# Kernel optimization log

Measured on AMD Instinct MI355X. Metric: run time of the kernel, lower is better.

The kernel has to match this reference:

```python
import jax, jax.numpy as jnp
import numpy as np

N, E, D, H, C = 50000, 800000, 128, 128, 40
EPS = 1e-5


def setup_inputs() -> dict:
    key = jax.random.key(0)
    ks = jax.random.split(key, 18)
    s = lambda d: 1.0 / np.sqrt(d)
    inp = {
        "x": jax.random.normal(ks[0], (N, D), dtype=jnp.float32),
        "edge_index": jax.random.randint(ks[1], (2, E), 0, N, dtype=jnp.int64),
        # GCNConv weights (x @ W + b after normalized aggregation)
        "W1": jax.random.normal(ks[2], (D, H), dtype=jnp.float32) * s(D),
        "b1": jax.random.normal(ks[3], (H,), dtype=jnp.float32) * 0.01,
        "W2": jax.random.normal(ks[4], (H, H), dtype=jnp.float32) * s(H),
        "b2": jax.random.normal(ks[5], (H,), dtype=jnp.float32) * 0.01,
        "W3": jax.random.normal(ks[6], (H, H), dtype=jnp.float32) * s(H),
        "b3": jax.random.normal(ks[7], (H,), dtype=jnp.float32) * 0.01,
        # LayerNorm params (applied after layers 0 and 1 only)
        "ln1_g": 1.0 + 0.1 * jax.random.normal(ks[8], (H,), dtype=jnp.float32),
        "ln1_b": 0.1 * jax.random.normal(ks[9], (H,), dtype=jnp.float32),
        "ln2_g": 1.0 + 0.1 * jax.random.normal(ks[10], (H,), dtype=jnp.float32),
        "ln2_b": 0.1 * jax.random.normal(ks[11], (H,), dtype=jnp.float32),
        # post_mp MLP head
        "mpW1": jax.random.normal(ks[12], (H, H), dtype=jnp.float32) * s(H),
        "mpb1": jax.random.normal(ks[13], (H,), dtype=jnp.float32) * 0.01,
        "mpW2": jax.random.normal(ks[14], (H, C), dtype=jnp.float32) * s(H),
        "mpb2": jax.random.normal(ks[15], (C,), dtype=jnp.float32) * 0.01,
    }
    return inp


def _layernorm(h, g, b):
    mu = jnp.mean(h, axis=-1, keepdims=True)
    var = jnp.mean((h - mu) ** 2, axis=-1, keepdims=True)
    return (h - mu) * jax.lax.rsqrt(var + EPS) * g + b


def _gcn_forward(x, edge_index, params):
    (W1, b1, W2, b2, W3, b3, ln1_g, ln1_b, ln2_g, ln2_b, mpW1, mpb1, mpW2, mpb2) = params
    n = x.shape[0]
    loop = jnp.arange(n, dtype=edge_index.dtype)
    src = jnp.concatenate([edge_index[0], loop])  # source-to-target flow + self-loops
    dst = jnp.concatenate([edge_index[1], loop])
    deg = jax.ops.segment_sum(jnp.ones_like(src, dtype=x.dtype), dst, num_segments=n)
    dis = jax.lax.rsqrt(deg)  # deg >= 1 due to self-loops
    norm = dis[src] * dis[dst]  # [E+N]

    def conv(h, W, b):
        h = h @ W
        msg = h[src] * norm[:, None]  # gather + scale
        return jax.ops.segment_sum(msg, dst, num_segments=n) + b  # scatter-add

    h = x
    # layer 0
    h = conv(h, W1, b1)
    h = jax.nn.relu(h)  # dropout p=0.1 -> identity in eval
    h = _layernorm(h, ln1_g, ln1_b)
    # layer 1
    h = conv(h, W2, b2)
    h = jax.nn.relu(h)
    h = _layernorm(h, ln2_g, ln2_b)
    # layer 2 (emb is pre-relu conv output)
    emb = conv(h, W3, b3)
    h = jax.nn.relu(emb)
    # post_mp: Linear -> Dropout(eval: identity) -> Linear
    h = h @ mpW1 + mpb1
    logits = h @ mpW2 + mpb2
    return emb, jax.nn.log_softmax(logits, axis=1)


def reference(x, edge_index, W1, b1, W2, b2, W3, b3, ln1_g, ln1_b, ln2_g, ln2_b, mpW1, mpb1, mpW2, mpb2):
    params = (W1, b1, W2, b2, W3, b3, ln1_g, ln1_b, ln2_g, ln2_b, mpW1, mpb1, mpW2, mpb2)
    return _gcn_forward(x, edge_index, params)
```

## Files before the change

kernel.cpp:

```cpp
#include <hip/hip_runtime.h>

typedef __bf16 bf16x8 __attribute__((ext_vector_type(8)));
typedef float  f32x4  __attribute__((ext_vector_type(4)));
typedef float  f32x2  __attribute__((ext_vector_type(2)));
typedef unsigned short u16;
typedef unsigned int   u32;
typedef long long      i64;

#define BSH  7
#define BCAP 4096
#define NPB  256

__device__ __forceinline__ float b2f(u16 x){ return __uint_as_float(((u32)x) << 16); }
__device__ __forceinline__ u16 f2b(float x){
  u32 u = __float_as_uint(x);
  return (u16)((u + 0x7FFFu + ((u >> 16) & 1u)) >> 16);
}

__device__ __forceinline__ void d2acc(u32 pair, f32x2& a){
  f32x2 t;
  t.x = __uint_as_float(pair << 16);
  t.y = __uint_as_float(pair & 0xFFFF0000u);
  a += t;
}
__device__ __forceinline__ void acc8(uint4 q, f32x2* a){
  d2acc(q.x, a[0]); d2acc(q.y, a[1]); d2acc(q.z, a[2]); d2acc(q.w, a[3]);
}

__global__ __launch_bounds__(256) void k_detect(const u16* __restrict__ x,
                                                const u32* __restrict__ ei,
                                                int* __restrict__ flags,
                                                u16* __restrict__ T, int n){
  __shared__ int sh[2];
  int t = threadIdx.x;
  if (t < 2) sh[t] = 0;
  __syncthreads();
  int sane = 0;
  for (int i = t; i < 4096; i += 256){
    u16 u = x[i]; u32 e = (u >> 7) & 0xFFu;
    if (u == 0 || (e >= 0x70u && e <= 0x8Fu)) sane++;
  }
  int nz = 0;
  for (int i = t; i < 1024; i += 256)
    if (ei[2*i + 1] != 0u) nz++;
  atomicAdd(&sh[0], sane);
  atomicAdd(&sh[1], nz);
  if (t < 128) T[(size_t)n*128 + t] = 0;
  else         T[(size_t)n*128 + t] = 0;
  __syncthreads();
  if (t == 0){
    flags[0] = (sh[0] < 3500) ? 1 : 0;
    flags[1] = (sh[1] == 0) ? 1 : 0;
  }
}

__device__ __forceinline__ int ld_idx(const void* ei, long long j, int is64){
  return is64 ? (int)((const i64*)ei)[j] : ((const int*)ei)[j];
}
__device__ __forceinline__ void ld8(const void* p, int base, int f, float* o){
  if (f){
    float4 a = *(const float4*)((const float*)p + base);
    float4 b = *(const float4*)((const float*)p + base + 4);
    o[0]=a.x; o[1]=a.y; o[2]=a.z; o[3]=a.w;
    o[4]=b.x; o[5]=b.y; o[6]=b.z; o[7]=b.w;
  } else {
    uint4 q = *(const uint4*)((const u16*)p + base);
    o[0]=b2f((u16)(q.x&0xffff)); o[1]=b2f((u16)(q.x>>16));
    o[2]=b2f((u16)(q.y&0xffff)); o[3]=b2f((u16)(q.y>>16));
    o[4]=b2f((u16)(q.z&0xffff)); o[5]=b2f((u16)(q.z>>16));
    o[6]=b2f((u16)(q.w&0xffff)); o[7]=b2f((u16)(q.w>>16));
  }
}

__global__ __launch_bounds__(256) void k_partA(const void* __restrict__ ei, int E, int n,
                                               int* __restrict__ cntmat,
                                               const int* __restrict__ flags, int nbuk){
  __shared__ int cnt[512];
  int t = threadIdx.x;
  int is64 = flags[1];
  for (int i = t; i < 512; i += 256) cnt[i] = 0;
  __syncthreads();
  long long R = ((long long)E + NPB - 1) / NPB;
  long long lo = (long long)blockIdx.x * R;
  long long hi = lo + R; if (hi > E) hi = E;
  for (long long e = lo + t; e < hi; e += 256){
    int d = ld_idx(ei, (long long)E + e, is64);
    if ((unsigned)d < (unsigned)n) atomicAdd(&cnt[(unsigned)d >> BSH], 1);
  }
  __syncthreads();
  for (int b = t; b < nbuk; b += 256)
    cntmat[(size_t)b*NPB + blockIdx.x] = cnt[b];
}

__global__ __launch_bounds__(NPB) void k_scanBK(const int* __restrict__ cntmat,
                                                int* __restrict__ basemat,
                                                int* __restrict__ bcnt){
  __shared__ int sh[NPB];
  int b = blockIdx.x, t = threadIdx.x;
  int v = cntmat[(size_t)b*NPB + t];
  sh[t] = v; __syncthreads();
  for (int off = 1; off < NPB; off <<= 1){
    int u = 0; if (t >= off) u = sh[t - off];
    __syncthreads(); sh[t] += u; __syncthreads();
  }
  basemat[(size_t)b*NPB + t] = sh[t] - v;
  if (t == NPB-1) bcnt[b] = sh[t];
}

__global__ __launch_bounds__(256) void k_partC(const void* __restrict__ ei, int E, int n,
                                               const int* __restrict__ basemat,
                                               u32* __restrict__ ebuf,
                                               const int* __restrict__ flags, int nbuk){
  __shared__ int cur[512];
  int t = threadIdx.x;
  int is64 = flags[1];
  for (int i = t; i < 512; i += 256) cur[i] = 0;
  __syncthreads();
  for (int b = t; b < nbuk; b += 256) cur[b] = basemat[(size_t)b*NPB + blockIdx.x];
  __syncthreads();
  long long R = ((long long)E + NPB - 1) / NPB;
  long long lo = (long long)blockIdx.x * R;
  long long hi = lo + R; if (hi > E) hi = E;
  for (long long e = lo + t; e < hi; e += 256){
    int d = ld_idx(ei, (long long)E + e, is64);
    int s = ld_idx(ei, e, is64);
    if ((unsigned)d < (unsigned)n && (unsigned)s < (unsigned)n){
      int b = (unsigned)d >> BSH;
      int p = atomicAdd(&cur[b], 1);
      if (p < BCAP) ebuf[(size_t)b*BCAP + p] = (u32)s | ((u32)(d & ((1<<BSH)-1)) << 17);
    }
  }
}

__global__ __launch_bounds__(256) void k_bdeg(const int* __restrict__ bcnt,
                                              const u32* __restrict__ ebuf,
                                              int* __restrict__ deg, int n){
  __shared__ int cnt[1<<BSH];
  int b = blockIdx.x, t = threadIdx.x;
  if (t < (1<<BSH)) cnt[t] = 0;
  __syncthreads();
  int m = bcnt[b]; if (m > BCAP) m = BCAP;
  const u32* eb = ebuf + (size_t)b*BCAP;
  for (int i = t; i < m; i += 256)
    atomicAdd(&cnt[eb[i] >> 17], 1);
  __syncthreads();
  if (t < (1<<BSH)){
    int node = (b << BSH) + t;
    if (node < n) deg[node] = cnt[t];
  }
}

__global__ __launch_bounds__(256) void k_scanA(const int* __restrict__ deg, int n,
                                               int* __restrict__ bsum){
  __shared__ int sh[256];
  int t = threadIdx.x;
  int base = blockIdx.x*1024 + t*4;
  int s = 0;
  #pragma unroll
  for (int i = 0; i < 4; ++i){
    int idx = base + i;
    if (idx < n) s += (deg[idx] + 3) & ~3;
  }
  sh[t] = s; __syncthreads();
  for (int off = 128; off; off >>= 1){
    if (t < off) sh[t] += sh[t + off];
    __syncthreads();
  }
  if (t == 0) bsum[blockIdx.x] = sh[0];
}

__global__ __launch_bounds__(256) void k_scanB(int* __restrict__ bsum, int nB,
                                               int* __restrict__ rowptr, int n){
  __shared__ int sh[256];
  int t = threadIdx.x;
  int v = (t < nB) ? bsum[t] : 0;
  sh[t] = v; __syncthreads();
  for (int off = 1; off < 256; off <<= 1){
    int u = 0; if (t >= off) u = sh[t - off];
    __syncthreads(); sh[t] += u; __syncthreads();
  }
  if (t < nB) bsum[t] = sh[t] - v;
  if (t == 255) rowptr[n] = sh[255];
}

__global__ __launch_bounds__(256) void k_scanC(const int* __restrict__ deg, int n,
                                               const int* __restrict__ bsum,
                                               int* __restrict__ rowptr,
                                               float* __restrict__ dis){
  __shared__ int sh[256];
  int t = threadIdx.x;
  int base = blockIdx.x*1024 + t*4;
  int d[4]; int s = 0;
  #pragma unroll
  for (int i = 0; i < 4; ++i){
    int idx = base + i;
    d[i] = (idx < n) ? deg[idx] : 0;
    s += (d[i] + 3) & ~3;
  }
  sh[t] = s; __syncthreads();
  for (int off = 1; off < 256; off <<= 1){
    int u = 0; if (t >= off) u = sh[t - off];
    __syncthreads(); sh[t] += u; __syncthreads();
  }
  int run = bsum[blockIdx.x] + sh[t] - s;
  #pragma unroll
  for (int i = 0; i < 4; ++i){
    int idx = base + i;
    if (idx < n){
      rowptr[idx] = run; run += (d[i] + 3) & ~3;
      dis[idx] = rsqrtf((float)(d[i] + 1));
    }
  }
}

__global__ __launch_bounds__(256) void k_bfill(const int* __restrict__ bcnt,
                                               const u32* __restrict__ ebuf,
                                               const int* __restrict__ rowptr,
                                               int* __restrict__ colx, int n){
  __shared__ int cur[1<<BSH];
  int b = blockIdx.x, t = threadIdx.x;
  int node = (b << BSH) + (t & ((1<<BSH)-1));
  if (t < (1<<BSH))
    cur[t] = (node < n) ? rowptr[node] : 0;
  __syncthreads();
  int m = bcnt[b]; if (m > BCAP) m = BCAP;
  const u32* eb = ebuf + (size_t)b*BCAP;
  for (int i = t; i < m; i += 256){
    u32 e = eb[i];
    int p = atomicAdd(&cur[e >> 17], 1);
    colx[p] = (int)((e & 0x1FFFFu) << 8);
  }
  __syncthreads();
  if (t < (1<<BSH) && node < n){
    int zoff = n << 8;
    int end = rowptr[node + 1];
    for (int p = cur[t]; p < end; ++p) colx[p] = zoff;
  }
}

__global__ __launch_bounds__(64) void k_shufW3(const void* __restrict__ W1,
                                               const void* __restrict__ W2,
                                               const void* __restrict__ W3,
                                               u16* __restrict__ Ws,
                                               const int* __restrict__ flags){
  int f = flags[0];
  int sel = blockIdx.x >> 5;
  const void* W = (sel == 0) ? W1 : (sel == 1) ? W2 : W3;
  u16* Wo = Ws + (size_t)sel * 128 * 128;
  int bid = blockIdx.x & 31;
  int nt = bid >> 2, kk = bid & 3;
  int l = threadIdx.x;
  int g = l >> 4, mr = l & 15;
  int nn = nt*16 + mr;
  #pragma unroll
  for (int i = 0; i < 8; ++i){
    int k = kk*32 + g*4 + (i & 3) + ((i >> 2) << 4);
    u16 w = f ? f2b(((const float*)W)[k*128 + nn]) : ((const u16*)W)[k*128 + nn];
    Wo[(size_t)(bid*64 + l)*8 + i] = w;
  }
}

__global__ __launch_bounds__(256) void k_gemm(const void* __restrict__ A, int aExt,
    const u16* __restrict__ Ws, const float* __restrict__ dis,
    u16* __restrict__ T, int nTiles, const int* __restrict__ flags)
{
  int wave = threadIdx.x >> 6, lane = threadIdx.x & 63;
  int tile = blockIdx.x*4 + wave;
  if (tile >= nTiles) return;
  int g = lane >> 4, mr = lane & 15;
  int f = aExt ? flags[0] : 0;
  union U8 { ushort4 q[2]; u16 s[8]; bf16x8 b; };
  bf16x8 a[4];
  if (f){
    const float* ap = (const float*)A + (size_t)(tile*16 + mr)*128;
    #pragma unroll
    for (int kk = 0; kk < 4; ++kk){
      float4 p = *(const float4*)(ap + kk*32 + g*4);
      float4 q = *(const float4*)(ap + kk*32 + g*4 + 16);
      U8 u;
      u.s[0]=f2b(p.x); u.s[1]=f2b(p.y); u.s[2]=f2b(p.z); u.s[3]=f2b(p.w);
      u.s[4]=f2b(q.x); u.s[5]=f2b(q.y); u.s[6]=f2b(q.z); u.s[7]=f2b(q.w);
      a[kk] = u.b;
    }
  } else {
    const u16* ap = (const u16*)A + (size_t)(tile*16 + mr)*128;
    #pragma unroll
    for (int kk = 0; kk < 4; ++kk){
      U8 u;
      u.q[0] = *(const ushort4*)(ap + kk*32 + g*4);
      u.q[1] = *(const ushort4*)(ap + kk*32 + g*4 + 16);
      a[kk] = u.b;
    }
  }
  float dj[4];
  #pragma unroll
  for (int j = 0; j < 4; ++j) dj[j] = dis[tile*16 + g*4 + j];
  #pragma unroll
  for (int nt = 0; nt < 8; ++nt){
    f32x4 acc = {0.f,0.f,0.f,0.f};
    #pragma unroll
    for (int kk = 0; kk < 4; ++kk){
      bf16x8 b = *(const bf16x8*)(Ws + (size_t)((nt*4 + kk)*64 + lane)*8);
      acc = __builtin_amdgcn_mfma_f32_16x16x32_bf16(a[kk], b, acc, 0, 0, 0);
    }
    int nn = nt*16 + mr;
    #pragma unroll
    for (int j = 0; j < 4; ++j){
      int row = tile*16 + g*4 + j;
      T[(size_t)row*128 + nn] = f2b(acc[j] * dj[j]);
    }
  }
}

template<int MODE>
__global__ __launch_bounds__(256) void k_agg(const u16* __restrict__ T,
    const int* __restrict__ rowptr, const int* __restrict__ colx,
    const float* __restrict__ dis, const void* __restrict__ bias,
    const void* __restrict__ lg, const void* __restrict__ lb,
    void* __restrict__ outA, int n, const int* __restrict__ flags)
{
  int wave = threadIdx.x >> 6, l = threadIdx.x & 63;
  int g = l >> 4, c = l & 15;
  int v = blockIdx.x*16 + wave*4 + g;
  bool alive = v < n;
  int vv = alive ? v : (n - 1);
  int f = flags[0];
  const char* Tb = (const char*)T + c*16;

  f32x2 aA[4] = {};
  f32x2 aB[4] = {};
  {
    uint4 q = *(const uint4*)(Tb + ((size_t)vv << 8));
    acc8(q, aA);
  }
  int s = rowptr[vv], e = rowptr[vv+1];
  int i = s;
  for (; i + 8 <= e; i += 8){
    uint4 oA = *(const uint4*)(colx + i);
    uint4 oB = *(const uint4*)(colx + i + 4);
    uint4 q0 = *(const uint4*)(Tb + oA.x);
    uint4 q1 = *(const uint4*)(Tb + oA.y);
    uint4 q2 = *(const uint4*)(Tb + oA.z);
    uint4 q3 = *(const uint4*)(Tb + oA.w);
    uint4 q4 = *(const uint4*)(Tb + oB.x);
    uint4 q5 = *(const uint4*)(Tb + oB.y);
    uint4 q6 = *(const uint4*)(Tb + oB.z);
    uint4 q7 = *(const uint4*)(Tb + oB.w);
    acc8(q0, aA); acc8(q1, aB); acc8(q2, aA); acc8(q3, aB);
    acc8(q4, aA); acc8(q5, aB); acc8(q6, aA); acc8(q7, aB);
  }
  if (i < e){
    uint4 o = *(const uint4*)(colx + i);
    uint4 q0 = *(const uint4*)(Tb + o.x);
    uint4 q1 = *(const uint4*)(Tb + o.y);
    uint4 q2 = *(const uint4*)(Tb + o.z);
    uint4 q3 = *(const uint4*)(Tb + o.w);
    acc8(q0, aA); acc8(q1, aB); acc8(q2, aA); acc8(q3, aB);
  }

  float acc[8];
  #pragma unroll
  for (int k = 0; k < 4; ++k){
    acc[2*k]   = aA[k].x + aB[k].x;
    acc[2*k+1] = aA[k].y + aB[k].y;
  }
  float sc = dis[vv];
  float bv[8]; ld8(bias, c*8, f, bv);
  float x[8];
  #pragma unroll
  for (int k = 0; k < 8; ++k) x[k] = fmaf(acc[k], sc, bv[k]);

  if (MODE == 0){
    #pragma unroll
    for (int k = 0; k < 8; ++k) x[k] = fmaxf(x[k], 0.f);
    float sum = 0.f;
    #pragma unroll
    for (int k = 0; k < 8; ++k) sum += x[k];
    #pragma unroll
    for (int off = 8; off; off >>= 1) sum += __shfl_xor(sum, off);
    float mu = sum * (1.f/128.f);
    float vs = 0.f;
    #pragma unroll
    for (int k = 0; k < 8; ++k){ float d = x[k] - mu; vs += d*d; }
    #pragma unroll
    for (int off = 8; off; off >>= 1) vs += __shfl_xor(vs, off);
    float inv = rsqrtf(vs*(1.f/128.f) + 1e-5f);
    float gv[8], bvv[8];
    ld8(lg, c*8, f, gv); ld8(lb, c*8, f, bvv);
    if (alive){
      uint4 w;
      float y0,y1;
      y0 = (x[0]-mu)*inv*gv[0] + bvv[0]; y1 = (x[1]-mu)*inv*gv[1] + bvv[1];
      w.x = (u32)f2b(y0) | ((u32)f2b(y1) << 16);
      y0 = (x[2]-mu)*inv*gv[2] + bvv[2]; y1 = (x[3]-mu)*inv*gv[3] + bvv[3];
      w.y = (u32)f2b(y0) | ((u32)f2b(y1) << 16);
      y0 = (x[4]-mu)*inv*gv[4] + bvv[4]; y1 = (x[5]-mu)*inv*gv[5] + bvv[5];
      w.z = (u32)f2b(y0) | ((u32)f2b(y1) << 16);
      y0 = (x[6]-mu)*inv*gv[6] + bvv[6]; y1 = (x[7]-mu)*inv*gv[7] + bvv[7];
      w.w = (u32)f2b(y0) | ((u32)f2b(y1) << 16);
      *(uint4*)((u16*)outA + (size_t)v*128 + c*8) = w;
    }
  } else {
    if (alive){
      if (f){
        float* oa = (float*)outA + (size_t)v*128 + c*8;
        *(float4*)(oa)     = make_float4(x[0], x[1], x[2], x[3]);
        *(float4*)(oa + 4) = make_float4(x[4], x[5], x[6], x[7]);
      } else {
        uint4 w;
        w.x = (u32)f2b(x[0]) | ((u32)f2b(x[1]) << 16);
        w.y = (u32)f2b(x[2]) | ((u32)f2b(x[3]) << 16);
        w.z = (u32)f2b(x[4]) | ((u32)f2b(x[5]) << 16);
        w.w = (u32)f2b(x[6]) | ((u32)f2b(x[7]) << 16);
        *(uint4*)((u16*)outA + (size_t)v*128 + c*8) = w;
      }
    }
  }
}

__global__ __launch_bounds__(128) void k_wc(const void* __restrict__ mpW1, const void* __restrict__ mpb1,
    const void* __restrict__ mpW2, const void* __restrict__ mpb2,
    float* __restrict__ Wc, float* __restrict__ bc, const int* __restrict__ flags)
{
  int f = flags[0];
  int c = blockIdx.x;
  int k = threadIdx.x;
  float acc = 0.f;
  if (f){
    const float* A  = (const float*)mpW1 + (size_t)k*128;
    const float* B2 = (const float*)mpW2;
    #pragma unroll 8
    for (int j = 0; j < 128; ++j) acc = fmaf(A[j], B2[j*40 + c], acc);
    if (k == 0){
      const float* b1p = (const float*)mpb1;
      float b = ((const float*)mpb2)[c];
      #pragma unroll 8
      for (int j = 0; j < 128; ++j) b = fmaf(b1p[j], B2[j*40 + c], b);
      bc[c] = b;
    }
  } else {
    const u16* A  = (const u16*)mpW1 + (size_t)k*128;
    const u16* B2 = (const u16*)mpW2;
    #pragma unroll 8
    for (int j = 0; j < 128; ++j) acc = fmaf(b2f(A[j]), b2f(B2[j*40 + c]), acc);
    if (k == 0){
      const u16* b1p = (const u16*)mpb1;
      float b = b2f(((const u16*)mpb2)[c]);
      #pragma unroll 8
      for (int j = 0; j < 128; ++j) b = fmaf(b2f(b1p[j]), b2f(B2[j*40 + c]), b);
      bc[c] = b;
    }
  }
  Wc[k*40 + c] = acc;
}

__global__ __launch_bounds__(64) void k_shufWc(const float* __restrict__ Wc, u16* __restrict__ Wcs){
  int bid = blockIdx.x;
  int nt = bid >> 2, kk = bid & 3;
  int l = threadIdx.x;
  int g = l >> 4, mr = l & 15;
  int nn = nt*16 + mr;
  #pragma unroll
  for (int i = 0; i < 8; ++i){
    int k = kk*32 + g*4 + (i & 3) + ((i >> 2) << 4);
    Wcs[(size_t)(bid*64 + l)*8 + i] = (nn < 40) ? f2b(Wc[k*40 + nn]) : (u16)0;
  }
}

__global__ __launch_bounds__(256) void k_logitsM(const u16* __restrict__ Wcs,
    const float* __restrict__ bc, void* __restrict__ dout, int n,
    const int* __restrict__ flags)
{
  int wave = threadIdx.x >> 6, lane = threadIdx.x & 63;
  int tile = blockIdx.x*4 + wave;
  int nTiles = n >> 4;
  if (tile >= nTiles) return;
  int f = flags[0];
  int g = lane >> 4, mr = lane & 15;
  union U8 { ushort4 q[2]; u16 s[8]; bf16x8 b; };
  bf16x8 a[4];
  if (f){
    const float* ap = (const float*)dout + (size_t)(tile*16 + mr)*128;
    #pragma unroll
    for (int kk = 0; kk < 4; ++kk){
      float4 p = *(const float4*)(ap + kk*32 + g*4);
      float4 q = *(const float4*)(ap + kk*32 + g*4 + 16);
      U8 u;
      u.s[0]=f2b(fmaxf(p.x,0.f)); u.s[1]=f2b(fmaxf(p.y,0.f));
      u.s[2]=f2b(fmaxf(p.z,0.f)); u.s[3]=f2b(fmaxf(p.w,0.f));
      u.s[4]=f2b(fmaxf(q.x,0.f)); u.s[5]=f2b(fmaxf(q.y,0.f));
      u.s[6]=f2b(fmaxf(q.z,0.f)); u.s[7]=f2b(fmaxf(q.w,0.f));
      a[kk] = u.b;
    }
  } else {
    const u16* ap = (const u16*)dout + (size_t)(tile*16 + mr)*128;
    #pragma unroll
    for (int kk = 0; kk < 4; ++kk){
      U8 u;
      u.q[0] = *(const ushort4*)(ap + kk*32 + g*4);
      u.q[1] = *(const ushort4*)(ap + kk*32 + g*4 + 16);
      #pragma unroll
      for (int i = 0; i < 8; ++i) u.s[i] = (u.s[i] & 0x8000u) ? (u16)0 : u.s[i];
      a[kk] = u.b;
    }
  }
  f32x4 acc[3];
  #pragma unroll
  for (int nt = 0; nt < 3; ++nt){
    f32x4 c4 = {0.f,0.f,0.f,0.f};
    #pragma unroll
    for (int kk = 0; kk < 4; ++kk){
      bf16x8 b = *(const bf16x8*)(Wcs + (size_t)((nt*4 + kk)*64 + lane)*8);
      c4 = __builtin_amdgcn_mfma_f32_16x16x32_bf16(a[kk], b, c4, 0, 0, 0);
    }
    acc[nt] = c4;
  }
  float bcv[3]; bool valid[3];
  #pragma unroll
  for (int nt = 0; nt < 3; ++nt){
    int c = nt*16 + mr;
    valid[nt] = (c < 40);
    bcv[nt] = valid[nt] ? bc[c] : 0.f;
  }
  float* of = (float*)dout + (size_t)n*128;
  u16*  ob = (u16*) dout + (size_t)n*128;
  #pragma unroll
  for (int j = 0; j < 4; ++j){
    float l0 = valid[0] ? acc[0][j] + bcv[0] : -3.0e38f;
    float l1 = valid[1] ? acc[1][j] + bcv[1] : -3.0e38f;
    float l2 = valid[2] ? acc[2][j] + bcv[2] : -3.0e38f;
    float m = fmaxf(l0, fmaxf(l1, l2));
    #pragma unroll
    for (int off = 8; off; off >>= 1) m = fmaxf(m, __shfl_xor(m, off));
    float ssum = (valid[0] ? expf(l0 - m) : 0.f)
               + (valid[1] ? expf(l1 - m) : 0.f)
               + (valid[2] ? expf(l2 - m) : 0.f);
    #pragma unroll
    for (int off = 8; off; off >>= 1) ssum += __shfl_xor(ssum, off);
    float lgs = m + logf(ssum);
    int node = tile*16 + g*4 + j;
    #pragma unroll
    for (int nt = 0; nt < 3; ++nt){
      if (valid[nt]){
        int c = nt*16 + mr;
        float r = (nt==0 ? l0 : (nt==1 ? l1 : l2)) - lgs;
        if (f) of[(size_t)node*40 + c] = r;
        else   ob[(size_t)node*40 + c] = f2b(r);
      }
    }
  }
}

extern "C" void kernel_launch(void* const* d_in, const int* in_sizes, int n_in,
                              void* d_out, int out_size, void* d_ws, size_t ws_size,
                              hipStream_t stream)
{
  const int n = in_sizes[0] / 128;
  const int E = in_sizes[1] / 2;

  const void* x    = d_in[0];
  const void* ei   = d_in[1];
  const void* W1   = d_in[2];
  const void* b1   = d_in[3];
  const void* W2   = d_in[4];
  const void* b2   = d_in[5];
  const void* W3   = d_in[6];
  const void* b3   = d_in[7];
  const void* ln1g = d_in[8];
  const void* ln1b = d_in[9];
  const void* ln2g = d_in[10];
  const void* ln2b = d_in[11];
  const void* mpW1 = d_in[12];
  const void* mpb1 = d_in[13];
  const void* mpW2 = d_in[14];
  const void* mpb2 = d_in[15];

  u16* Hbuf = (u16*)d_out;

  char* w = (char*)d_ws;
  size_t off = 0;
  auto alloc = [&](size_t bytes)->char*{
    char* p = w + off; off = (off + bytes + 255) & ~(size_t)255; return p;
  };
  const int nbuk = (n + (1<<BSH) - 1) >> BSH;

  int*   flags = (int*)  alloc(256);
  float* dis   = (float*)alloc((size_t)n*4);
  int*   deg   = (int*)  alloc((size_t)n*4);
  int*   rowp  = (int*)  alloc((size_t)(n+1)*4);
  int*   bsum  = (int*)  alloc(1024);
  int*   bcnt  = (int*)  alloc((size_t)nbuk*4);
  int*   cntm  = (int*)  alloc((size_t)nbuk*NPB*4);
  int*   basem = (int*)  alloc((size_t)nbuk*NPB*4);
  u32*   ebuf  = (u32*)  alloc((size_t)nbuk*BCAP*4);
  int*   colx  = (int*)  alloc(((size_t)E + 4*(size_t)n)*4 + 256);
  u16*   T     = (u16*)  alloc((size_t)(n+1)*128*2);
  u16*   Ws    = (u16*)  alloc((size_t)3*128*128*2);
  float* Wc    = (float*)alloc((size_t)128*40*4);
  float* bc    = (float*)alloc((size_t)64*4);
  u16*   Wcs   = (u16*)  alloc((size_t)12*64*8*2);

  int nB = (n + 1023) / 1024;

  k_detect<<<1, 256, 0, stream>>>((const u16*)x, (const u32*)ei, flags, T, n);
  k_shufW3<<<96, 64, 0, stream>>>(W1, W2, W3, Ws, flags);
  k_partA <<<NPB, 256, 0, stream>>>(ei, E, n, cntm, flags, nbuk);
  k_scanBK<<<nbuk, NPB, 0, stream>>>(cntm, basem, bcnt);
  k_partC <<<NPB, 256, 0, stream>>>(ei, E, n, basem, ebuf, flags, nbuk);
  k_bdeg  <<<nbuk, 256, 0, stream>>>(bcnt, ebuf, deg, n);
  k_scanA <<<nB, 256, 0, stream>>>(deg, n, bsum);
  k_scanB <<<1, 256, 0, stream>>>(bsum, nB, rowp, n);
  k_scanC <<<nB, 256, 0, stream>>>(deg, n, bsum, rowp, dis);
  k_bfill <<<nbuk, 256, 0, stream>>>(bcnt, ebuf, rowp, colx, n);
  k_wc    <<<40, 128, 0, stream>>>(mpW1, mpb1, mpW2, mpb2, Wc, bc, flags);
  k_shufWc<<<12, 64, 0, stream>>>(Wc, Wcs);

  int nTiles = (n + 15) / 16;
  int gG = (nTiles + 3) / 4;
  int gA = (n + 15) / 16;

  k_gemm <<<gG, 256, 0, stream>>>(x, 1, Ws, dis, T, nTiles, flags);
  k_agg<0><<<gA, 256, 0, stream>>>(T, rowp, colx, dis, b1, ln1g, ln1b, Hbuf, n, flags);
  k_gemm <<<gG, 256, 0, stream>>>(Hbuf, 0, Ws + (size_t)128*128, dis, T, nTiles, flags);
  k_agg<0><<<gA, 256, 0, stream>>>(T, rowp, colx, dis, b2, ln2g, ln2b, Hbuf, n, flags);
  k_gemm <<<gG, 256, 0, stream>>>(Hbuf, 0, Ws + (size_t)2*128*128, dis, T, nTiles, flags);
  k_agg<1><<<gA, 256, 0, stream>>>(T, rowp, colx, dis, b3, nullptr, nullptr, d_out, n, flags);
  k_logitsM<<<gG, 256, 0, stream>>>(Wcs, bc, d_out, n, flags);
}
```

Baseline: 213.3 us.

## Sub-bucket edges by source-node range to sort CSR columns by source

Edge partitioning now keys each edge by destination bucket and by a source-node range (8192-node tiles). The CSR column lists are therefore filled in roughly source-sorted order, which should give the aggregation gathers better locality across neighbouring rows. In exchange, the bucket count grows several-fold, so the scan needs more blocks and the count and fill kernels loop over sub-buckets, with one extra barrier per sub-bucket. The per-bucket capacity drops to 512, which risks dropping edges if a sub-bucket overflows.

```diff
diff --git a/kernel.cpp b/kernel.cpp
--- a/kernel.cpp
+++ b/kernel.cpp
@@ -7,9 +7,11 @@
 typedef unsigned int   u32;
 typedef long long      i64;
 
-#define BSH  7
-#define BCAP 4096
-#define NPB  256
+#define BSH   7
+#define SRCSH 13
+#define BCAP  512
+#define NPB   256
+#define MAXB2 4096
 
 __device__ __forceinline__ float b2f(u16 x){ return __uint_as_float(((u32)x) << 16); }
 __device__ __forceinline__ u16 f2b(float x){
@@ -46,7 +48,6 @@
   atomicAdd(&sh[0], sane);
   atomicAdd(&sh[1], nz);
   if (t < 128) T[(size_t)n*128 + t] = 0;
-  else         T[(size_t)n*128 + t] = 0;
   __syncthreads();
   if (t == 0){
     flags[0] = (sh[0] < 3500) ? 1 : 0;
@@ -74,21 +75,26 @@
 
 __global__ __launch_bounds__(256) void k_partA(const void* __restrict__ ei, int E, int n,
                                                int* __restrict__ cntmat,
-                                               const int* __restrict__ flags, int nbuk){
-  __shared__ int cnt[512];
+                                               const int* __restrict__ flags,
+                                               int NT, int nb2){
+  __shared__ int cnt[MAXB2];
   int t = threadIdx.x;
   int is64 = flags[1];
-  for (int i = t; i < 512; i += 256) cnt[i] = 0;
+  for (int i = t; i < nb2; i += 256) cnt[i] = 0;
   __syncthreads();
   long long R = ((long long)E + NPB - 1) / NPB;
   long long lo = (long long)blockIdx.x * R;
   long long hi = lo + R; if (hi > E) hi = E;
   for (long long e = lo + t; e < hi; e += 256){
     int d = ld_idx(ei, (long long)E + e, is64);
-    if ((unsigned)d < (unsigned)n) atomicAdd(&cnt[(unsigned)d >> BSH], 1);
-  }
-  __syncthreads();
-  for (int b = t; b < nbuk; b += 256)
+    int s = ld_idx(ei, e, is64);
+    if ((unsigned)d < (unsigned)n && (unsigned)s < (unsigned)n){
+      int key = ((unsigned)d >> BSH)*NT + ((unsigned)s >> SRCSH);
+      atomicAdd(&cnt[key], 1);
+    }
+  }
+  __syncthreads();
+  for (int b = t; b < nb2; b += 256)
     cntmat[(size_t)b*NPB + blockIdx.x] = cnt[b];
 }
 
@@ -110,13 +116,12 @@
 __global__ __launch_bounds__(256) void k_partC(const void* __restrict__ ei, int E, int n,
                                                const int* __restrict__ basemat,
                                                u32* __restrict__ ebuf,
-                                               const int* __restrict__ flags, int nbuk){
-  __shared__ int cur[512];
+                                               const int* __restrict__ flags,
+                                               int NT, int nb2){
+  __shared__ int cur[MAXB2];
   int t = threadIdx.x;
   int is64 = flags[1];
-  for (int i = t; i < 512; i += 256) cur[i] = 0;
-  __syncthreads();
-  for (int b = t; b < nbuk; b += 256) cur[b] = basemat[(size_t)b*NPB + blockIdx.x];
+  for (int b = t; b < nb2; b += 256) cur[b] = basemat[(size_t)b*NPB + blockIdx.x];
   __syncthreads();
   long long R = ((long long)E + NPB - 1) / NPB;
   long long lo = (long long)blockIdx.x * R;
@@ -125,24 +130,27 @@
     int d = ld_idx(ei, (long long)E + e, is64);
     int s = ld_idx(ei, e, is64);
     if ((unsigned)d < (unsigned)n && (unsigned)s < (unsigned)n){
-      int b = (unsigned)d >> BSH;
-      int p = atomicAdd(&cur[b], 1);
-      if (p < BCAP) ebuf[(size_t)b*BCAP + p] = (u32)s | ((u32)(d & ((1<<BSH)-1)) << 17);
+      int key = ((unsigned)d >> BSH)*NT + ((unsigned)s >> SRCSH);
+      int p = atomicAdd(&cur[key], 1);
+      if (p < BCAP) ebuf[(size_t)key*BCAP + p] = (u32)s | ((u32)(d & ((1<<BSH)-1)) << 17);
     }
   }
 }
 
 __global__ __launch_bounds__(256) void k_bdeg(const int* __restrict__ bcnt,
                                               const u32* __restrict__ ebuf,
-                                              int* __restrict__ deg, int n){
+                                              int* __restrict__ deg, int n, int NT){
   __shared__ int cnt[1<<BSH];
   int b = blockIdx.x, t = threadIdx.x;
   if (t < (1<<BSH)) cnt[t] = 0;
   __syncthreads();
-  int m = bcnt[b]; if (m > BCAP) m = BCAP;
-  const u32* eb = ebuf + (size_t)b*BCAP;
-  for (int i = t; i < m; i += 256)
-    atomicAdd(&cnt[eb[i] >> 17], 1);
+  for (int st = 0; st < NT; ++st){
+    int key = b*NT + st;
+    int m = bcnt[key]; if (m > BCAP) m = BCAP;
+    const u32* eb = ebuf + (size_t)key*BCAP;
+    for (int i = t; i < m; i += 256)
+      atomicAdd(&cnt[eb[i] >> 17], 1);
+  }
   __syncthreads();
   if (t < (1<<BSH)){
     int node = (b << BSH) + t;
@@ -216,21 +224,24 @@
 __global__ __launch_bounds__(256) void k_bfill(const int* __restrict__ bcnt,
                                                const u32* __restrict__ ebuf,
                                                const int* __restrict__ rowptr,
-                                               int* __restrict__ colx, int n){
+                                               int* __restrict__ colx, int n, int NT){
   __shared__ int cur[1<<BSH];
   int b = blockIdx.x, t = threadIdx.x;
   int node = (b << BSH) + (t & ((1<<BSH)-1));
   if (t < (1<<BSH))
     cur[t] = (node < n) ? rowptr[node] : 0;
   __syncthreads();
-  int m = bcnt[b]; if (m > BCAP) m = BCAP;
-  const u32* eb = ebuf + (size_t)b*BCAP;
-  for (int i = t; i < m; i += 256){
-    u32 e = eb[i];
-    int p = atomicAdd(&cur[e >> 17], 1);
-    colx[p] = (int)((e & 0x1FFFFu) << 8);
-  }
-  __syncthreads();
+  for (int st = 0; st < NT; ++st){
+    int key = b*NT + st;
+    int m = bcnt[key]; if (m > BCAP) m = BCAP;
+    const u32* eb = ebuf + (size_t)key*BCAP;
+    for (int i = t; i < m; i += 256){
+      u32 e = eb[i];
+      int p = atomicAdd(&cur[e >> 17], 1);
+      colx[p] = (int)((e & 0x1FFFFu) << 8);
+    }
+    __syncthreads();
+  }
   if (t < (1<<BSH) && node < n){
     int zoff = n << 8;
     int end = rowptr[node + 1];
@@ -583,16 +594,19 @@
     char* p = w + off; off = (off + bytes + 255) & ~(size_t)255; return p;
   };
   const int nbuk = (n + (1<<BSH) - 1) >> BSH;
+  int NT = (n + (1<<SRCSH) - 1) >> SRCSH;
+  int nb2 = nbuk * NT;
+  if (nb2 > MAXB2){ NT = MAXB2 / nbuk; nb2 = nbuk * NT; }
 
   int*   flags = (int*)  alloc(256);
   float* dis   = (float*)alloc((size_t)n*4);
   int*   deg   = (int*)  alloc((size_t)n*4);
   int*   rowp  = (int*)  alloc((size_t)(n+1)*4);
   int*   bsum  = (int*)  alloc(1024);
-  int*   bcnt  = (int*)  alloc((size_t)nbuk*4);
-  int*   cntm  = (int*)  alloc((size_t)nbuk*NPB*4);
-  int*   basem = (int*)  alloc((size_t)nbuk*NPB*4);
-  u32*   ebuf  = (u32*)  alloc((size_t)nbuk*BCAP*4);
+  int*   bcnt  = (int*)  alloc((size_t)nb2*4);
+  int*   cntm  = (int*)  alloc((size_t)nb2*NPB*4);
+  int*   basem = (int*)  alloc((size_t)nb2*NPB*4);
+  u32*   ebuf  = (u32*)  alloc((size_t)nb2*BCAP*4);
   int*   colx  = (int*)  alloc(((size_t)E + 4*(size_t)n)*4 + 256);
   u16*   T     = (u16*)  alloc((size_t)(n+1)*128*2);
   u16*   Ws    = (u16*)  alloc((size_t)3*128*128*2);
@@ -604,14 +618,14 @@
 
   k_detect<<<1, 256, 0, stream>>>((const u16*)x, (const u32*)ei, flags, T, n);
   k_shufW3<<<96, 64, 0, stream>>>(W1, W2, W3, Ws, flags);
-  k_partA <<<NPB, 256, 0, stream>>>(ei, E, n, cntm, flags, nbuk);
-  k_scanBK<<<nbuk, NPB, 0, stream>>>(cntm, basem, bcnt);
-  k_partC <<<NPB, 256, 0, stream>>>(ei, E, n, basem, ebuf, flags, nbuk);
-  k_bdeg  <<<nbuk, 256, 0, stream>>>(bcnt, ebuf, deg, n);
+  k_partA <<<NPB, 256, 0, stream>>>(ei, E, n, cntm, flags, NT, nb2);
+  k_scanBK<<<nb2, NPB, 0, stream>>>(cntm, basem, bcnt);
+  k_partC <<<NPB, 256, 0, stream>>>(ei, E, n, basem, ebuf, flags, NT, nb2);
+  k_bdeg  <<<nbuk, 256, 0, stream>>>(bcnt, ebuf, deg, n, NT);
   k_scanA <<<nB, 256, 0, stream>>>(deg, n, bsum);
   k_scanB <<<1, 256, 0, stream>>>(bsum, nB, rowp, n);
   k_scanC <<<nB, 256, 0, stream>>>(deg, n, bsum, rowp, dis);
-  k_bfill <<<nbuk, 256, 0, stream>>>(bcnt, ebuf, rowp, colx, n);
+  k_bfill <<<nbuk, 256, 0, stream>>>(bcnt, ebuf, rowp, colx, n, NT);
   k_wc    <<<40, 128, 0, stream>>>(mpW1, mpb1, mpW2, mpb2, Wc, bc, flags);
   k_shufWc<<<12, 64, 0, stream>>>(Wc, Wcs);
 
```

New measurement: 227.2 us. +6.5%, slower.

## Fold CSR prefix scan into bucket kernels and merge Wc shuffle

Applied to the files above, without the earlier changes.

Replaces the three-kernel scan over per-node degrees (scanA/scanB/scanC) with a per-bucket reduction inside k_bdeg, a single 512-thread bucket scan, and an intra-bucket scan inside k_bfill, which now also writes rowptr and dis. The Wc precompute writes the shuffled bf16 layout directly, which removes the separate k_shufWc launch and the intermediate buffer. The aim is to cut several small kernel launches and global round trips in the preprocessing chain. It relies on nbuk being at most 512 so the single-block scan is valid.

```diff
diff --git a/kernel.cpp b/kernel.cpp
--- a/kernel.cpp
+++ b/kernel.cpp
@@ -46,7 +46,6 @@
   atomicAdd(&sh[0], sane);
   atomicAdd(&sh[1], nz);
   if (t < 128) T[(size_t)n*128 + t] = 0;
-  else         T[(size_t)n*128 + t] = 0;
   __syncthreads();
   if (t == 0){
     flags[0] = (sh[0] < 3500) ? 1 : 0;
@@ -134,8 +133,10 @@
 
 __global__ __launch_bounds__(256) void k_bdeg(const int* __restrict__ bcnt,
                                               const u32* __restrict__ ebuf,
-                                              int* __restrict__ deg, int n){
+                                              int* __restrict__ deg,
+                                              int* __restrict__ bksum, int n){
   __shared__ int cnt[1<<BSH];
+  __shared__ int red[1<<BSH];
   int b = blockIdx.x, t = threadIdx.x;
   if (t < (1<<BSH)) cnt[t] = 0;
   __syncthreads();
@@ -144,84 +145,70 @@
   for (int i = t; i < m; i += 256)
     atomicAdd(&cnt[eb[i] >> 17], 1);
   __syncthreads();
+  int node = (b << BSH) + t;
   if (t < (1<<BSH)){
-    int node = (b << BSH) + t;
-    if (node < n) deg[node] = cnt[t];
-  }
-}
-
-__global__ __launch_bounds__(256) void k_scanA(const int* __restrict__ deg, int n,
-                                               int* __restrict__ bsum){
-  __shared__ int sh[256];
+    int d = (node < n) ? cnt[t] : 0;
+    if (node < n) deg[node] = d;
+    red[t] = (d + 3) & ~3;
+  }
+  __syncthreads();
+  for (int off = 64; off; off >>= 1){
+    if (t < off) red[t] += red[t + off];
+    __syncthreads();
+  }
+  if (t == 0) bksum[b] = red[0];
+}
+
+__global__ __launch_bounds__(512) void k_scanBkt(const int* __restrict__ bksum,
+                                                 int* __restrict__ bkbase,
+                                                 int* __restrict__ rowptr,
+                                                 int nbuk, int n){
+  __shared__ int sh[512];
   int t = threadIdx.x;
-  int base = blockIdx.x*1024 + t*4;
-  int s = 0;
-  #pragma unroll
-  for (int i = 0; i < 4; ++i){
-    int idx = base + i;
-    if (idx < n) s += (deg[idx] + 3) & ~3;
-  }
-  sh[t] = s; __syncthreads();
-  for (int off = 128; off; off >>= 1){
-    if (t < off) sh[t] += sh[t + off];
-    __syncthreads();
-  }
-  if (t == 0) bsum[blockIdx.x] = sh[0];
-}
-
-__global__ __launch_bounds__(256) void k_scanB(int* __restrict__ bsum, int nB,
-                                               int* __restrict__ rowptr, int n){
-  __shared__ int sh[256];
-  int t = threadIdx.x;
-  int v = (t < nB) ? bsum[t] : 0;
+  int v = (t < nbuk) ? bksum[t] : 0;
   sh[t] = v; __syncthreads();
-  for (int off = 1; off < 256; off <<= 1){
+  for (int off = 1; off < 512; off <<= 1){
     int u = 0; if (t >= off) u = sh[t - off];
     __syncthreads(); sh[t] += u; __syncthreads();
   }
-  if (t < nB) bsum[t] = sh[t] - v;
-  if (t == 255) rowptr[n] = sh[255];
-}
-
-__global__ __launch_bounds__(256) void k_scanC(const int* __restrict__ deg, int n,
-                                               const int* __restrict__ bsum,
-                                               int* __restrict__ rowptr,
-                                               float* __restrict__ dis){
-  __shared__ int sh[256];
-  int t = threadIdx.x;
-  int base = blockIdx.x*1024 + t*4;
-  int d[4]; int s = 0;
-  #pragma unroll
-  for (int i = 0; i < 4; ++i){
-    int idx = base + i;
-    d[i] = (idx < n) ? deg[idx] : 0;
-    s += (d[i] + 3) & ~3;
-  }
-  sh[t] = s; __syncthreads();
-  for (int off = 1; off < 256; off <<= 1){
-    int u = 0; if (t >= off) u = sh[t - off];
-    __syncthreads(); sh[t] += u; __syncthreads();
-  }
-  int run = bsum[blockIdx.x] + sh[t] - s;
-  #pragma unroll
-  for (int i = 0; i < 4; ++i){
-    int idx = base + i;
-    if (idx < n){
-      rowptr[idx] = run; run += (d[i] + 3) & ~3;
-      dis[idx] = rsqrtf((float)(d[i] + 1));
-    }
-  }
+  if (t < nbuk) bkbase[t] = sh[t] - v;
+  if (t == 511) rowptr[n] = sh[511];
 }
 
 __global__ __launch_bounds__(256) void k_bfill(const int* __restrict__ bcnt,
                                                const u32* __restrict__ ebuf,
-                                               const int* __restrict__ rowptr,
+                                               const int* __restrict__ deg,
+                                               const int* __restrict__ bkbase,
+                                               int* __restrict__ rowptr,
+                                               float* __restrict__ dis,
                                                int* __restrict__ colx, int n){
   __shared__ int cur[1<<BSH];
+  __shared__ int pdv[1<<BSH];
+  __shared__ int base_[1<<BSH];
   int b = blockIdx.x, t = threadIdx.x;
-  int node = (b << BSH) + (t & ((1<<BSH)-1));
-  if (t < (1<<BSH))
-    cur[t] = (node < n) ? rowptr[node] : 0;
+  int node = (b << BSH) + t;
+  int d = 0, pd = 0;
+  if (t < (1<<BSH)){
+    d = (node < n) ? deg[node] : 0;
+    pd = (d + 3) & ~3;
+    pdv[t] = pd;
+    if (node < n) dis[node] = rsqrtf((float)(d + 1));
+  }
+  __syncthreads();
+  if (t < (1<<BSH)) base_[t] = pdv[t];
+  __syncthreads();
+  for (int off = 1; off < (1<<BSH); off <<= 1){
+    int u = 0;
+    if (t < (1<<BSH) && t >= off) u = base_[t - off];
+    __syncthreads();
+    if (t < (1<<BSH)) base_[t] += u;
+    __syncthreads();
+  }
+  if (t < (1<<BSH)){
+    int myBase = bkbase[b] + base_[t] - pdv[t];
+    if (node < n) rowptr[node] = myBase;
+    cur[t] = myBase;
+  }
   __syncthreads();
   int m = bcnt[b]; if (m > BCAP) m = BCAP;
   const u32* eb = ebuf + (size_t)b*BCAP;
@@ -233,7 +220,7 @@
   __syncthreads();
   if (t < (1<<BSH) && node < n){
     int zoff = n << 8;
-    int end = rowptr[node + 1];
+    int end = (bkbase[b] + base_[t] - pdv[t]) + pd;
     for (int p = cur[t]; p < end; ++p) colx[p] = zoff;
   }
 }
@@ -420,51 +407,45 @@
 
 __global__ __launch_bounds__(128) void k_wc(const void* __restrict__ mpW1, const void* __restrict__ mpb1,
     const void* __restrict__ mpW2, const void* __restrict__ mpb2,
-    float* __restrict__ Wc, float* __restrict__ bc, const int* __restrict__ flags)
+    u16* __restrict__ Wcs, float* __restrict__ bc, const int* __restrict__ flags)
 {
   int f = flags[0];
   int c = blockIdx.x;
   int k = threadIdx.x;
   float acc = 0.f;
-  if (f){
-    const float* A  = (const float*)mpW1 + (size_t)k*128;
-    const float* B2 = (const float*)mpW2;
-    #pragma unroll 8
-    for (int j = 0; j < 128; ++j) acc = fmaf(A[j], B2[j*40 + c], acc);
-    if (k == 0){
-      const float* b1p = (const float*)mpb1;
-      float b = ((const float*)mpb2)[c];
+  if (c < 40){
+    if (f){
+      const float* A  = (const float*)mpW1 + (size_t)k*128;
+      const float* B2 = (const float*)mpW2;
       #pragma unroll 8
-      for (int j = 0; j < 128; ++j) b = fmaf(b1p[j], B2[j*40 + c], b);
-      bc[c] = b;
-    }
-  } else {
-    const u16* A  = (const u16*)mpW1 + (size_t)k*128;
-    const u16* B2 = (const u16*)mpW2;
-    #pragma unroll 8
-    for (int j = 0; j < 128; ++j) acc = fmaf(b2f(A[j]), b2f(B2[j*40 + c]), acc);
-    if (k == 0){
-      const u16* b1p = (const u16*)mpb1;
-      float b = b2f(((const u16*)mpb2)[c]);
+      for (int j = 0; j < 128; ++j) acc = fmaf(A[j], B2[j*40 + c], acc);
+      if (k == 0){
+        const float* b1p = (const float*)mpb1;
+        float b = ((const float*)mpb2)[c];
+        #pragma unroll 8
+        for (int j = 0; j < 128; ++j) b = fmaf(b1p[j], B2[j*40 + c], b);
+        bc[c] = b;
+      }
+    } else {
+      const u16* A  = (const u16*)mpW1 + (size_t)k*128;
+      const u16* B2 = (const u16*)mpW2;
       #pragma unroll 8
-      for (int j = 0; j < 128; ++j) b = fmaf(b2f(b1p[j]), b2f(B2[j*40 + c]), b);
-      bc[c] = b;
-    }
-  }
-  Wc[k*40 + c] = acc;
-}
-
-__global__ __launch_bounds__(64) void k_shufWc(const float* __restrict__ Wc, u16* __restrict__ Wcs){
-  int bid = blockIdx.x;
-  int nt = bid >> 2, kk = bid & 3;
-  int l = threadIdx.x;
-  int g = l >> 4, mr = l & 15;
-  int nn = nt*16 + mr;
-  #pragma unroll
-  for (int i = 0; i < 8; ++i){
-    int k = kk*32 + g*4 + (i & 3) + ((i >> 2) << 4);
-    Wcs[(size_t)(bid*64 + l)*8 + i] = (nn < 40) ? f2b(Wc[k*40 + nn]) : (u16)0;
-  }
+      for (int j = 0; j < 128; ++j) acc = fmaf(b2f(A[j]), b2f(B2[j*40 + c]), acc);
+      if (k == 0){
+        const u16* b1p = (const u16*)mpb1;
+        float b = b2f(((const u16*)mpb2)[c]);
+        #pragma unroll 8
+        for (int j = 0; j < 128; ++j) b = fmaf(b2f(b1p[j]), b2f(B2[j*40 + c]), b);
+        bc[c] = b;
+      }
+    }
+  }
+  int kk = k >> 5, rem = k & 31;
+  int g = (rem & 15) >> 2;
+  int i = ((rem >> 4) << 2) | (rem & 3);
+  int bid = (c >> 4)*4 + kk;
+  int l = (g << 4) | (c & 15);
+  Wcs[(size_t)(bid*64 + l)*8 + i] = (c < 40) ? f2b(acc) : (u16)0;
 }
 
 __global__ __launch_bounds__(256) void k_logitsM(const u16* __restrict__ Wcs,
@@ -588,7 +569,8 @@
   float* dis   = (float*)alloc((size_t)n*4);
   int*   deg   = (int*)  alloc((size_t)n*4);
   int*   rowp  = (int*)  alloc((size_t)(n+1)*4);
-  int*   bsum  = (int*)  alloc(1024);
+  int*   bksum = (int*)  alloc((size_t)nbuk*4 + 256);
+  int*   bkbase= (int*)  alloc((size_t)nbuk*4 + 256);
   int*   bcnt  = (int*)  alloc((size_t)nbuk*4);
   int*   cntm  = (int*)  alloc((size_t)nbuk*NPB*4);
   int*   basem = (int*)  alloc((size_t)nbuk*NPB*4);
@@ -596,24 +578,18 @@
   int*   colx  = (int*)  alloc(((size_t)E + 4*(size_t)n)*4 + 256);
   u16*   T     = (u16*)  alloc((size_t)(n+1)*128*2);
   u16*   Ws    = (u16*)  alloc((size_t)3*128*128*2);
-  float* Wc    = (float*)alloc((size_t)128*40*4);
   float* bc    = (float*)alloc((size_t)64*4);
   u16*   Wcs   = (u16*)  alloc((size_t)12*64*8*2);
-
-  int nB = (n + 1023) / 1024;
 
   k_detect<<<1, 256, 0, stream>>>((const u16*)x, (const u32*)ei, flags, T, n);
   k_shufW3<<<96, 64, 0, stream>>>(W1, W2, W3, Ws, flags);
   k_partA <<<NPB, 256, 0, stream>>>(ei, E, n, cntm, flags, nbuk);
   k_scanBK<<<nbuk, NPB, 0, stream>>>(cntm, basem, bcnt);
   k_partC <<<NPB, 256, 0, stream>>>(ei, E, n, basem, ebuf, flags, nbuk);
-  k_bdeg  <<<nbuk, 256, 0, stream>>>(bcnt, ebuf, deg, n);
-  k_scanA <<<nB, 256, 0, stream>>>(deg, n, bsum);
-  k_scanB <<<1, 256, 0, stream>>>(bsum, nB, rowp, n);
-  k_scanC <<<nB, 256, 0, stream>>>(deg, n, bsum, rowp, dis);
-  k_bfill <<<nbuk, 256, 0, stream>>>(bcnt, ebuf, rowp, colx, n);
-  k_wc    <<<40, 128, 0, stream>>>(mpW1, mpb1, mpW2, mpb2, Wc, bc, flags);
-  k_shufWc<<<12, 64, 0, stream>>>(Wc, Wcs);
+  k_bdeg  <<<nbuk, 256, 0, stream>>>(bcnt, ebuf, deg, bksum, n);
+  k_scanBkt<<<1, 512, 0, stream>>>(bksum, bkbase, rowp, nbuk, n);
+  k_bfill <<<nbuk, 256, 0, stream>>>(bcnt, ebuf, deg, bkbase, rowp, dis, colx, n);
+  k_wc    <<<48, 128, 0, stream>>>(mpW1, mpb1, mpW2, mpb2, Wcs, bc, flags);
 
   int nTiles = (n + 15) / 16;
   int gG = (nTiles + 3) / 4;
```

New measurement: 206.2 us. -3.3%, faster.
